# Kernel optimization log

Hardware: AMD Instinct MI355X
Metric: run time of the kernel (lower is better)

The kernel has to match this reference:

```python
import jax, jax.numpy as jnp
import numpy as np

D = 1024
N = 64
EPS = 1e-6


def setup_inputs() -> dict:
    key = jax.random.key(0)
    ks = jax.random.split(key, 10)
    sD = 1.0 / np.sqrt(D)
    sN = 1.0 / np.sqrt(N)
    x = jax.random.normal(ks[0], (8, 4096, D), dtype=jnp.float32)
    A_log = jax.random.normal(ks[1], (N,), dtype=jnp.float32)
    WB = jax.random.uniform(ks[2], (N, D), jnp.float32, -sD, sD)
    bB = jax.random.uniform(ks[3], (N,), jnp.float32, -sD, sD)
    WC = jax.random.uniform(ks[4], (N, D), jnp.float32, -sD, sD)
    bC = jax.random.uniform(ks[5], (N,), jnp.float32, -sD, sD)
    Wd = jax.random.uniform(ks[6], (1, D), jnp.float32, -sD, sD)
    bd = jax.random.uniform(ks[7], (1,), jnp.float32, -sD, sD)
    Wo = jax.random.uniform(ks[8], (D, N), jnp.float32, -sN, sN)
    bo = jax.random.uniform(ks[9], (D,), jnp.float32, -sN, sN)
    return {"x": x, "A_log": A_log, "WB": WB, "bB": bB, "WC": WC, "bC": bC,
            "Wd": Wd, "bd": bd, "Wo": Wo, "bo": bo}


def reference(x, A_log, WB, bB, WC, bC, Wd, bd, Wo, bo):
    # x: (B, L, D)
    A = -jax.nn.softplus(A_log)                       # (N,)
    B_t = jnp.einsum('bld,nd->bln', x, WB) + bB       # (B, L, N)
    _C_proj = jnp.einsum('bld,nd->bln', x, WC) + bC   # computed then overwritten in source (dead)
    Delta = jax.nn.softplus(jnp.einsum('bld,nd->bln', x, Wd) + bd)  # (B, L, 1)
    dA = jnp.exp(A * Delta)                           # (B, L, N)
    dB = (dA - 1.0) / (A + EPS) * B_t                 # (B, L, N)
    conv = jnp.cumprod(dA, axis=1)
    ones = jnp.ones_like(dA[:, :1, :])
    Ct = jnp.concatenate([ones, conv[:, :-1, :]], axis=1)  # shifted cumprod (replaces C_t)
    z = dB / (Ct + EPS)
    s = jnp.cumsum(z, axis=1)
    X_state = Ct * s                                  # x_init = 0
    Y = jnp.einsum('bln,dn->bld', Ct * X_state, Wo) + bo
    return Y
```

## Files before the change

kernel.cpp:

```cpp
#include <hip/hip_runtime.h>
#include <math.h>

#define DDIM 1024
#define NCH 64
#define LSEQ 4096
#define NBATCH 8
#define NROWS (NBATCH * LSEQ)
#define EPSF 1e-6f
#define NCK 64
#define CLEN 64

__device__ __forceinline__ float softplusf(float v) {
    return (v > 20.0f) ? v : log1pf(expf(v));
}

__global__ void prep_kernel(const float* __restrict__ Wo, float* __restrict__ WoT) {
    int id = blockIdx.x * 256 + threadIdx.x;
    int n = id >> 10;
    int d = id & (DDIM - 1);
    WoT[n * DDIM + d] = Wo[d * NCH + n];
}

#define MT_A 128
#define KT_A 32

__global__ __launch_bounds__(256) void proj_kernel(
        const float* __restrict__ x,
        const float* __restrict__ A_log,
        const float* __restrict__ WB,
        const float* __restrict__ bB,
        const float* __restrict__ Wd,
        const float* __restrict__ bd,
        float* __restrict__ dA_g,
        float* __restrict__ dB_g) {
    __shared__ float x_lds[MT_A][37];
    __shared__ float w_lds[KT_A][68];
    __shared__ float delta_lds[MT_A];
    __shared__ float a_lds[NCH];
    __shared__ float bb_lds[NCH];

    const int t  = threadIdx.x;
    const int ng = t & 7;
    const int rg = t >> 3;
    const int R0 = blockIdx.x * MT_A;

    if (t < NCH) {
        a_lds[t]  = -softplusf(A_log[t]);
        bb_lds[t] = bB[t];
    }

    float acc[4][8];
    #pragma unroll
    for (int i = 0; i < 4; i++)
        #pragma unroll
        for (int j = 0; j < 8; j++) acc[i][j] = 0.0f;
    float dpart = 0.0f;

    for (int k0 = 0; k0 < DDIM; k0 += KT_A) {
        __syncthreads();
        #pragma unroll
        for (int p = 0; p < 4; p++) {
            int row = p * 32 + (t >> 3);
            int c   = (t & 7) * 4;
            const float4 v = *reinterpret_cast<const float4*>(&x[(size_t)(R0 + row) * DDIM + k0 + c]);
            x_lds[row][c + 0] = v.x; x_lds[row][c + 1] = v.y;
            x_lds[row][c + 2] = v.z; x_lds[row][c + 3] = v.w;
        }
        #pragma unroll
        for (int p = 0; p < 2; p++) {
            int n = p * 32 + (t >> 3);
            int c = (t & 7) * 4;
            const float4 v = *reinterpret_cast<const float4*>(&WB[(size_t)n * DDIM + k0 + c]);
            w_lds[c + 0][n] = v.x; w_lds[c + 1][n] = v.y;
            w_lds[c + 2][n] = v.z; w_lds[c + 3][n] = v.w;
        }
        if (t < 8) {
            int c = t * 4;
            const float4 v = *reinterpret_cast<const float4*>(&Wd[k0 + c]);
            w_lds[c + 0][64] = v.x; w_lds[c + 1][64] = v.y;
            w_lds[c + 2][64] = v.z; w_lds[c + 3][64] = v.w;
        }
        __syncthreads();

        #pragma unroll 8
        for (int k = 0; k < KT_A; k++) {
            float xv[4];
            #pragma unroll
            for (int i = 0; i < 4; i++) xv[i] = x_lds[rg + 32 * i][k];
            const float4 w0 = *reinterpret_cast<const float4*>(&w_lds[k][ng * 8]);
            const float4 w1 = *reinterpret_cast<const float4*>(&w_lds[k][ng * 8 + 4]);
            const float wv[8] = {w0.x, w0.y, w0.z, w0.w, w1.x, w1.y, w1.z, w1.w};
            #pragma unroll
            for (int i = 0; i < 4; i++)
                #pragma unroll
                for (int j = 0; j < 8; j++)
                    acc[i][j] = fmaf(xv[i], wv[j], acc[i][j]);
        }
        if (t < MT_A) {
            #pragma unroll 8
            for (int k = 0; k < KT_A; k++)
                dpart = fmaf(x_lds[t][k], w_lds[k][64], dpart);
        }
    }

    if (t < MT_A) delta_lds[t] = softplusf(dpart + bd[0]);
    __syncthreads();

    #pragma unroll
    for (int i = 0; i < 4; i++) {
        const int row   = rg + 32 * i;
        const float dlt = delta_lds[row];
        float oA[8], oB[8];
        #pragma unroll
        for (int j = 0; j < 8; j++) {
            const int n   = ng * 8 + j;
            const float a = a_lds[n];
            const float dAv = expf(a * dlt);
            const float Bt  = acc[i][j] + bb_lds[n];
            oA[j] = dAv;
            oB[j] = (dAv - 1.0f) / (a + EPSF) * Bt;
        }
        float* pA = &dA_g[(size_t)(R0 + row) * NCH + ng * 8];
        float* pB = &dB_g[(size_t)(R0 + row) * NCH + ng * 8];
        *reinterpret_cast<float4*>(pA)     = make_float4(oA[0], oA[1], oA[2], oA[3]);
        *reinterpret_cast<float4*>(pA + 4) = make_float4(oA[4], oA[5], oA[6], oA[7]);
        *reinterpret_cast<float4*>(pB)     = make_float4(oB[0], oB[1], oB[2], oB[3]);
        *reinterpret_cast<float4*>(pB + 4) = make_float4(oB[4], oB[5], oB[6], oB[7]);
    }
}


__global__ __launch_bounds__(64) void chunkprod_kernel(
        const float* __restrict__ dA_g, float* __restrict__ P) {
    const int n = threadIdx.x;
    const int blk = blockIdx.x;
    size_t base = (size_t)blk * CLEN * NCH + n;
    float p = 1.0f;
    #pragma unroll 8
    for (int u = 0; u < CLEN; u++) p *= dA_g[base + (size_t)u * NCH];
    P[(size_t)blk * NCH + n] = p;
}

__global__ __launch_bounds__(512) void stitch1_kernel(
        const float* __restrict__ P, float* __restrict__ E) {
    const int id = threadIdx.x;
    const int b = id >> 6, n = id & 63;
    size_t idx = (size_t)b * NCK * NCH + n;
    float e = 1.0f;
    for (int j = 0; j < NCK; j++) {
        E[idx + (size_t)j * NCH] = e;
        e *= P[idx + (size_t)j * NCH];
    }
}

__global__ __launch_bounds__(64) void chunkz_kernel(
        const float* __restrict__ dA_g, const float* __restrict__ dB_g,
        const float* __restrict__ E, float* __restrict__ Z) {
    const int n = threadIdx.x;
    const int blk = blockIdx.x;
    size_t base = (size_t)blk * CLEN * NCH + n;
    const float e = E[(size_t)blk * NCH + n];
    float L = 1.0f, zs = 0.0f;
    #pragma unroll 8
    for (int u = 0; u < CLEN; u++) {
        const float a  = dA_g[base + (size_t)u * NCH];
        const float bv = dB_g[base + (size_t)u * NCH];
        const float c  = e * L;
        zs += bv / (c + EPSF);
        L *= a;
    }
    Z[(size_t)blk * NCH + n] = zs;
}

__global__ __launch_bounds__(512) void stitch2_kernel(
        const float* __restrict__ Z, float* __restrict__ S) {
    const int id = threadIdx.x;
    const int b = id >> 6, n = id & 63;
    size_t idx = (size_t)b * NCK * NCH + n;
    float s = 0.0f;
    for (int j = 0; j < NCK; j++) {
        S[idx + (size_t)j * NCH] = s;
        s += Z[idx + (size_t)j * NCH];
    }
}

__global__ __launch_bounds__(64) void chunkout_kernel(
        const float* __restrict__ dA_g, float* __restrict__ dBG,
        const float* __restrict__ E, const float* __restrict__ S) {
    const int n = threadIdx.x;
    const int blk = blockIdx.x;
    size_t base = (size_t)blk * CLEN * NCH + n;
    const float e = E[(size_t)blk * NCH + n];
    float L = 1.0f;
    float s = S[(size_t)blk * NCH + n];
    #pragma unroll 8
    for (int u = 0; u < CLEN; u++) {
        const float a  = dA_g[base + (size_t)u * NCH];
        const float bv = dBG [base + (size_t)u * NCH];
        const float c  = e * L;
        s += bv / (c + EPSF);
        dBG[base + (size_t)u * NCH] = c * c * s;
        L *= a;
    }
}

#define MT_C 16
__global__ __launch_bounds__(256) void out_kernel(
        const float* __restrict__ G,
        const float* __restrict__ WoT,
        const float* __restrict__ bo,
        float* __restrict__ Y) {
    __shared__ float g_lds[NCH][20];
    const int t  = threadIdx.x;
    const int R0 = blockIdx.x * MT_C;

    {
        int row = t >> 4;
        int n4  = (t & 15) * 4;
        const float4 v = *reinterpret_cast<const float4*>(&G[(size_t)(R0 + row) * NCH + n4]);
        g_lds[n4 + 0][row] = v.x; g_lds[n4 + 1][row] = v.y;
        g_lds[n4 + 2][row] = v.z; g_lds[n4 + 3][row] = v.w;
    }
    __syncthreads();

    const int d0 = t * 4;
    float acc[MT_C][4];
    #pragma unroll
    for (int r = 0; r < MT_C; r++)
        #pragma unroll
        for (int j = 0; j < 4; j++) acc[r][j] = 0.0f;

    for (int n = 0; n < NCH; n++) {
        const float4 wo = *reinterpret_cast<const float4*>(&WoT[n * DDIM + d0]);
        float g[MT_C];
        #pragma unroll
        for (int q = 0; q < 4; q++) {
            const float4 gv = *reinterpret_cast<const float4*>(&g_lds[n][q * 4]);
            g[q * 4 + 0] = gv.x; g[q * 4 + 1] = gv.y;
            g[q * 4 + 2] = gv.z; g[q * 4 + 3] = gv.w;
        }
        #pragma unroll
        for (int r = 0; r < MT_C; r++) {
            acc[r][0] = fmaf(g[r], wo.x, acc[r][0]);
            acc[r][1] = fmaf(g[r], wo.y, acc[r][1]);
            acc[r][2] = fmaf(g[r], wo.z, acc[r][2]);
            acc[r][3] = fmaf(g[r], wo.w, acc[r][3]);
        }
    }

    const float4 bov = *reinterpret_cast<const float4*>(&bo[d0]);
    #pragma unroll
    for (int r = 0; r < MT_C; r++) {
        float4 o;
        o.x = acc[r][0] + bov.x; o.y = acc[r][1] + bov.y;
        o.z = acc[r][2] + bov.z; o.w = acc[r][3] + bov.w;
        *reinterpret_cast<float4*>(&Y[(size_t)(R0 + r) * DDIM + d0]) = o;
    }
}

extern "C" void kernel_launch(void* const* d_in, const int* in_sizes, int n_in,
                              void* d_out, int out_size, void* d_ws, size_t ws_size,
                              hipStream_t stream) {
    const float* x     = (const float*)d_in[0];
    const float* A_log = (const float*)d_in[1];
    const float* WB    = (const float*)d_in[2];
    const float* bB    = (const float*)d_in[3];
    const float* Wd    = (const float*)d_in[6];
    const float* bd    = (const float*)d_in[7];
    const float* Wo    = (const float*)d_in[8];
    const float* bo    = (const float*)d_in[9];
    float* Y = (float*)d_out;

    float* dA_g = (float*)d_ws;
    float* dBG  = dA_g + (size_t)NROWS * NCH;
    float* WoT  = dBG  + (size_t)NROWS * NCH;
    float* P    = WoT  + (size_t)NCH * DDIM;
    float* E    = P    + (size_t)NBATCH * NCK * NCH;
    float* Z    = E    + (size_t)NBATCH * NCK * NCH;
    float* S    = Z    + (size_t)NBATCH * NCK * NCH;

    const int NCHUNKS = NBATCH * NCK;

    prep_kernel<<<dim3(256), dim3(256), 0, stream>>>(Wo, WoT);
    proj_kernel<<<dim3(NROWS / MT_A), dim3(256), 0, stream>>>(
        x, A_log, WB, bB, Wd, bd, dA_g, dBG);
    chunkprod_kernel<<<dim3(NCHUNKS), dim3(64), 0, stream>>>(dA_g, P);
    stitch1_kernel<<<dim3(1), dim3(512), 0, stream>>>(P, E);
    chunkz_kernel<<<dim3(NCHUNKS), dim3(64), 0, stream>>>(dA_g, dBG, E, Z);
    stitch2_kernel<<<dim3(1), dim3(512), 0, stream>>>(Z, S);
    chunkout_kernel<<<dim3(NCHUNKS), dim3(64), 0, stream>>>(dA_g, dBG, E, S);
    out_kernel<<<dim3(NROWS / MT_C), dim3(256), 0, stream>>>(dBG, WoT, bo, Y);
}
```

Measured before the change: 459.5 us.

## Split-K projection with separate gate kernel, retile output GEMM, batch stitch loads

```diff
diff --git a/kernel.cpp b/kernel.cpp
--- a/kernel.cpp
+++ b/kernel.cpp
@@ -21,33 +21,25 @@
     WoT[n * DDIM + d] = Wo[d * NCH + n];
 }
 
-#define MT_A 128
-#define KT_A 32
-
-__global__ __launch_bounds__(256) void proj_kernel(
+#define MT 128
+#define KSPL 2
+#define KRNG (DDIM / KSPL)
+#define SUBK 32
+
+__global__ __launch_bounds__(256, 2) void proj2_kernel(
         const float* __restrict__ x,
-        const float* __restrict__ A_log,
         const float* __restrict__ WB,
-        const float* __restrict__ bB,
         const float* __restrict__ Wd,
-        const float* __restrict__ bd,
-        float* __restrict__ dA_g,
-        float* __restrict__ dB_g) {
-    __shared__ float x_lds[MT_A][37];
-    __shared__ float w_lds[KT_A][68];
-    __shared__ float delta_lds[MT_A];
-    __shared__ float a_lds[NCH];
-    __shared__ float bb_lds[NCH];
-
+        float* __restrict__ Bt0, float* __restrict__ Bt1,
+        float* __restrict__ De0, float* __restrict__ De1) {
+    __shared__ float x_lds[MT][36];
     const int t  = threadIdx.x;
-    const int ng = t & 7;
-    const int rg = t >> 3;
-    const int R0 = blockIdx.x * MT_A;
-
-    if (t < NCH) {
-        a_lds[t]  = -softplusf(A_log[t]);
-        bb_lds[t] = bB[t];
-    }
+    const int tr = t & 31;
+    const int tc = t >> 5;
+    const int rt = blockIdx.x >> 1;
+    const int ks = blockIdx.x & 1;
+    const int R0 = rt * MT;
+    const int kb0 = ks * KRNG;
 
     float acc[4][8];
     #pragma unroll
@@ -56,79 +48,76 @@
         for (int j = 0; j < 8; j++) acc[i][j] = 0.0f;
     float dpart = 0.0f;
 
-    for (int k0 = 0; k0 < DDIM; k0 += KT_A) {
+    for (int kk = 0; kk < KRNG; kk += SUBK) {
+        const int kb = kb0 + kk;
         __syncthreads();
         #pragma unroll
         for (int p = 0; p < 4; p++) {
-            int row = p * 32 + (t >> 3);
-            int c   = (t & 7) * 4;
-            const float4 v = *reinterpret_cast<const float4*>(&x[(size_t)(R0 + row) * DDIM + k0 + c]);
-            x_lds[row][c + 0] = v.x; x_lds[row][c + 1] = v.y;
-            x_lds[row][c + 2] = v.z; x_lds[row][c + 3] = v.w;
-        }
-        #pragma unroll
-        for (int p = 0; p < 2; p++) {
-            int n = p * 32 + (t >> 3);
-            int c = (t & 7) * 4;
-            const float4 v = *reinterpret_cast<const float4*>(&WB[(size_t)n * DDIM + k0 + c]);
-            w_lds[c + 0][n] = v.x; w_lds[c + 1][n] = v.y;
-            w_lds[c + 2][n] = v.z; w_lds[c + 3][n] = v.w;
-        }
-        if (t < 8) {
-            int c = t * 4;
-            const float4 v = *reinterpret_cast<const float4*>(&Wd[k0 + c]);
-            w_lds[c + 0][64] = v.x; w_lds[c + 1][64] = v.y;
-            w_lds[c + 2][64] = v.z; w_lds[c + 3][64] = v.w;
+            const int row = p * 32 + (t >> 3);
+            const int c   = (t & 7) * 4;
+            const float4 v = *reinterpret_cast<const float4*>(
+                &x[(size_t)(R0 + row) * DDIM + kb + c]);
+            *reinterpret_cast<float4*>(&x_lds[row][c]) = v;
         }
         __syncthreads();
 
-        #pragma unroll 8
-        for (int k = 0; k < KT_A; k++) {
-            float xv[4];
+        if (t < MT) {
+            #pragma unroll 8
+            for (int k = 0; k < SUBK; k++)
+                dpart = fmaf(x_lds[t][k], Wd[kb + k], dpart);
+        }
+
+        #pragma unroll
+        for (int k4 = 0; k4 < SUBK / 4; k4++) {
+            float4 wv[8];
             #pragma unroll
-            for (int i = 0; i < 4; i++) xv[i] = x_lds[rg + 32 * i][k];
-            const float4 w0 = *reinterpret_cast<const float4*>(&w_lds[k][ng * 8]);
-            const float4 w1 = *reinterpret_cast<const float4*>(&w_lds[k][ng * 8 + 4]);
-            const float wv[8] = {w0.x, w0.y, w0.z, w0.w, w1.x, w1.y, w1.z, w1.w};
+            for (int j = 0; j < 8; j++)
+                wv[j] = *reinterpret_cast<const float4*>(
+                    &WB[(size_t)(tc * 8 + j) * DDIM + kb + k4 * 4]);
+            float4 xv[4];
+            #pragma unroll
+            for (int i = 0; i < 4; i++)
+                xv[i] = *reinterpret_cast<const float4*>(&x_lds[tr + 32 * i][k4 * 4]);
             #pragma unroll
             for (int i = 0; i < 4; i++)
                 #pragma unroll
-                for (int j = 0; j < 8; j++)
-                    acc[i][j] = fmaf(xv[i], wv[j], acc[i][j]);
-        }
-        if (t < MT_A) {
-            #pragma unroll 8
-            for (int k = 0; k < KT_A; k++)
-                dpart = fmaf(x_lds[t][k], w_lds[k][64], dpart);
-        }
-    }
-
-    if (t < MT_A) delta_lds[t] = softplusf(dpart + bd[0]);
-    __syncthreads();
-
+                for (int j = 0; j < 8; j++) {
+                    acc[i][j] = fmaf(xv[i].x, wv[j].x, acc[i][j]);
+                    acc[i][j] = fmaf(xv[i].y, wv[j].y, acc[i][j]);
+                    acc[i][j] = fmaf(xv[i].z, wv[j].z, acc[i][j]);
+                    acc[i][j] = fmaf(xv[i].w, wv[j].w, acc[i][j]);
+                }
+        }
+    }
+
+    float* Bt = ks ? Bt1 : Bt0;
     #pragma unroll
     for (int i = 0; i < 4; i++) {
-        const int row   = rg + 32 * i;
-        const float dlt = delta_lds[row];
-        float oA[8], oB[8];
-        #pragma unroll
-        for (int j = 0; j < 8; j++) {
-            const int n   = ng * 8 + j;
-            const float a = a_lds[n];
-            const float dAv = expf(a * dlt);
-            const float Bt  = acc[i][j] + bb_lds[n];
-            oA[j] = dAv;
-            oB[j] = (dAv - 1.0f) / (a + EPSF) * Bt;
-        }
-        float* pA = &dA_g[(size_t)(R0 + row) * NCH + ng * 8];
-        float* pB = &dB_g[(size_t)(R0 + row) * NCH + ng * 8];
-        *reinterpret_cast<float4*>(pA)     = make_float4(oA[0], oA[1], oA[2], oA[3]);
-        *reinterpret_cast<float4*>(pA + 4) = make_float4(oA[4], oA[5], oA[6], oA[7]);
-        *reinterpret_cast<float4*>(pB)     = make_float4(oB[0], oB[1], oB[2], oB[3]);
-        *reinterpret_cast<float4*>(pB + 4) = make_float4(oB[4], oB[5], oB[6], oB[7]);
-    }
-}
-
+        const size_t base = (size_t)(R0 + tr + 32 * i) * NCH + tc * 8;
+        *reinterpret_cast<float4*>(&Bt[base])     = make_float4(acc[i][0], acc[i][1], acc[i][2], acc[i][3]);
+        *reinterpret_cast<float4*>(&Bt[base + 4]) = make_float4(acc[i][4], acc[i][5], acc[i][6], acc[i][7]);
+    }
+    if (t < MT) (ks ? De1 : De0)[R0 + t] = dpart;
+}
+
+__global__ __launch_bounds__(256) void gate_kernel(
+        const float* __restrict__ A_log, const float* __restrict__ bB,
+        const float* __restrict__ bd,
+        const float* __restrict__ De0, const float* __restrict__ De1,
+        float* __restrict__ dA_g,
+        float* __restrict__ dBG) {
+    const int t   = threadIdx.x;
+    const int n   = t & 63;
+    const int row = blockIdx.x * 4 + (t >> 6);
+    const size_t idx = (size_t)row * NCH + n;
+    const float a   = -softplusf(A_log[n]);
+    const float dlt = softplusf(De0[row] + De1[row] + bd[0]);
+    const float Btv = dBG[idx] + dA_g[idx] + bB[n];
+    const float dAv = expf(a * dlt);
+    const float dBv = (dAv - 1.0f) / (a + EPSF) * Btv;
+    dA_g[idx] = dAv;
+    dBG[idx]  = dBv;
+}
 
 __global__ __launch_bounds__(64) void chunkprod_kernel(
         const float* __restrict__ dA_g, float* __restrict__ P) {
@@ -147,9 +136,15 @@
     const int b = id >> 6, n = id & 63;
     size_t idx = (size_t)b * NCK * NCH + n;
     float e = 1.0f;
-    for (int j = 0; j < NCK; j++) {
-        E[idx + (size_t)j * NCH] = e;
-        e *= P[idx + (size_t)j * NCH];
+    for (int j0 = 0; j0 < NCK; j0 += 8) {
+        float p8[8];
+        #pragma unroll
+        for (int u = 0; u < 8; u++) p8[u] = P[idx + (size_t)(j0 + u) * NCH];
+        #pragma unroll
+        for (int u = 0; u < 8; u++) {
+            E[idx + (size_t)(j0 + u) * NCH] = e;
+            e *= p8[u];
+        }
     }
 }
 
@@ -178,9 +173,15 @@
     const int b = id >> 6, n = id & 63;
     size_t idx = (size_t)b * NCK * NCH + n;
     float s = 0.0f;
-    for (int j = 0; j < NCK; j++) {
-        S[idx + (size_t)j * NCH] = s;
-        s += Z[idx + (size_t)j * NCH];
+    for (int j0 = 0; j0 < NCK; j0 += 8) {
+        float z8[8];
+        #pragma unroll
+        for (int u = 0; u < 8; u++) z8[u] = Z[idx + (size_t)(j0 + u) * NCH];
+        #pragma unroll
+        for (int u = 0; u < 8; u++) {
+            S[idx + (size_t)(j0 + u) * NCH] = s;
+            s += z8[u];
+        }
     }
 }
 
@@ -204,57 +205,60 @@
     }
 }
 
-#define MT_C 16
-__global__ __launch_bounds__(256) void out_kernel(
+__global__ __launch_bounds__(256, 4) void out2_kernel(
         const float* __restrict__ G,
         const float* __restrict__ WoT,
         const float* __restrict__ bo,
         float* __restrict__ Y) {
-    __shared__ float g_lds[NCH][20];
+    __shared__ float g_lds[NCH][36];
     const int t  = threadIdx.x;
-    const int R0 = blockIdx.x * MT_C;
+    const int tc = t & 63;
+    const int tr = t >> 6;
+    const int R0 = (blockIdx.x >> 1) * 32;
+    const int D0 = (blockIdx.x & 1) * 512;
 
     {
-        int row = t >> 4;
-        int n4  = (t & 15) * 4;
-        const float4 v = *reinterpret_cast<const float4*>(&G[(size_t)(R0 + row) * NCH + n4]);
-        g_lds[n4 + 0][row] = v.x; g_lds[n4 + 1][row] = v.y;
-        g_lds[n4 + 2][row] = v.z; g_lds[n4 + 3][row] = v.w;
+        const int grow = t >> 3;
+        const int gn0  = (t & 7) * 8;
+        const float4 a0 = *reinterpret_cast<const float4*>(&G[(size_t)(R0 + grow) * NCH + gn0]);
+        const float4 a1 = *reinterpret_cast<const float4*>(&G[(size_t)(R0 + grow) * NCH + gn0 + 4]);
+        g_lds[gn0 + 0][grow] = a0.x; g_lds[gn0 + 1][grow] = a0.y;
+        g_lds[gn0 + 2][grow] = a0.z; g_lds[gn0 + 3][grow] = a0.w;
+        g_lds[gn0 + 4][grow] = a1.x; g_lds[gn0 + 5][grow] = a1.y;
+        g_lds[gn0 + 6][grow] = a1.z; g_lds[gn0 + 7][grow] = a1.w;
     }
     __syncthreads();
 
-    const int d0 = t * 4;
-    float acc[MT_C][4];
+    float acc[8][8];
     #pragma unroll
-    for (int r = 0; r < MT_C; r++)
-        #pragma unroll
-        for (int j = 0; j < 4; j++) acc[r][j] = 0.0f;
-
+    for (int i = 0; i < 8; i++)
+        #pragma unroll
+        for (int j = 0; j < 8; j++) acc[i][j] = 0.0f;
+
+    const size_t wcol = (size_t)D0 + tc * 8;
     for (int n = 0; n < NCH; n++) {
-        const float4 wo = *reinterpret_cast<const float4*>(&WoT[n * DDIM + d0]);
-        float g[MT_C];
-        #pragma unroll
-        for (int q = 0; q < 4; q++) {
-            const float4 gv = *reinterpret_cast<const float4*>(&g_lds[n][q * 4]);
-            g[q * 4 + 0] = gv.x; g[q * 4 + 1] = gv.y;
-            g[q * 4 + 2] = gv.z; g[q * 4 + 3] = gv.w;
-        }
-        #pragma unroll
-        for (int r = 0; r < MT_C; r++) {
-            acc[r][0] = fmaf(g[r], wo.x, acc[r][0]);
-            acc[r][1] = fmaf(g[r], wo.y, acc[r][1]);
-            acc[r][2] = fmaf(g[r], wo.z, acc[r][2]);
-            acc[r][3] = fmaf(g[r], wo.w, acc[r][3]);
-        }
-    }
-
-    const float4 bov = *reinterpret_cast<const float4*>(&bo[d0]);
+        const float4 g0 = *reinterpret_cast<const float4*>(&g_lds[n][tr * 8]);
+        const float4 g1 = *reinterpret_cast<const float4*>(&g_lds[n][tr * 8 + 4]);
+        const float4 w0 = *reinterpret_cast<const float4*>(&WoT[(size_t)n * DDIM + wcol]);
+        const float4 w1 = *reinterpret_cast<const float4*>(&WoT[(size_t)n * DDIM + wcol + 4]);
+        const float ga[8] = {g0.x, g0.y, g0.z, g0.w, g1.x, g1.y, g1.z, g1.w};
+        const float wa[8] = {w0.x, w0.y, w0.z, w0.w, w1.x, w1.y, w1.z, w1.w};
+        #pragma unroll
+        for (int i = 0; i < 8; i++)
+            #pragma unroll
+            for (int j = 0; j < 8; j++)
+                acc[i][j] = fmaf(ga[i], wa[j], acc[i][j]);
+    }
+
+    const float4 b0 = *reinterpret_cast<const float4*>(&bo[wcol]);
+    const float4 b1 = *reinterpret_cast<const float4*>(&bo[wcol + 4]);
     #pragma unroll
-    for (int r = 0; r < MT_C; r++) {
-        float4 o;
-        o.x = acc[r][0] + bov.x; o.y = acc[r][1] + bov.y;
-        o.z = acc[r][2] + bov.z; o.w = acc[r][3] + bov.w;
-        *reinterpret_cast<float4*>(&Y[(size_t)(R0 + r) * DDIM + d0]) = o;
+    for (int i = 0; i < 8; i++) {
+        const size_t yb = (size_t)(R0 + tr * 8 + i) * DDIM + wcol;
+        *reinterpret_cast<float4*>(&Y[yb]) =
+            make_float4(acc[i][0] + b0.x, acc[i][1] + b0.y, acc[i][2] + b0.z, acc[i][3] + b0.w);
+        *reinterpret_cast<float4*>(&Y[yb + 4]) =
+            make_float4(acc[i][4] + b1.x, acc[i][5] + b1.y, acc[i][6] + b1.z, acc[i][7] + b1.w);
     }
 }
 
@@ -278,16 +282,20 @@
     float* E    = P    + (size_t)NBATCH * NCK * NCH;
     float* Z    = E    + (size_t)NBATCH * NCK * NCH;
     float* S    = Z    + (size_t)NBATCH * NCK * NCH;
+    float* De0  = S    + (size_t)NBATCH * NCK * NCH;
+    float* De1  = De0  + (size_t)NROWS;
 
     const int NCHUNKS = NBATCH * NCK;
 
     prep_kernel<<<dim3(256), dim3(256), 0, stream>>>(Wo, WoT);
-    proj_kernel<<<dim3(NROWS / MT_A), dim3(256), 0, stream>>>(
-        x, A_log, WB, bB, Wd, bd, dA_g, dBG);
+    proj2_kernel<<<dim3((NROWS / MT) * KSPL), dim3(256), 0, stream>>>(
+        x, WB, Wd, dBG, dA_g, De0, De1);
+    gate_kernel<<<dim3(NROWS / 4), dim3(256), 0, stream>>>(
+        A_log, bB, bd, De0, De1, dA_g, dBG);
     chunkprod_kernel<<<dim3(NCHUNKS), dim3(64), 0, stream>>>(dA_g, P);
     stitch1_kernel<<<dim3(1), dim3(512), 0, stream>>>(P, E);
     chunkz_kernel<<<dim3(NCHUNKS), dim3(64), 0, stream>>>(dA_g, dBG, E, Z);
     stitch2_kernel<<<dim3(1), dim3(512), 0, stream>>>(Z, S);
     chunkout_kernel<<<dim3(NCHUNKS), dim3(64), 0, stream>>>(dA_g, dBG, E, S);
-    out_kernel<<<dim3(NROWS / MT_C), dim3(256), 0, stream>>>(dBG, WoT, bo, Y);
-}
+    out2_kernel<<<dim3((NROWS / 32) * 2), dim3(256), 0, stream>>>(dBG, WoT, bo, Y);
+}
```

After: 409.3 us. 10.9% less time.
